# Kernel tuning notes

Measured on AMD Instinct MI355X. Metric: run time of the kernel, lower is better.

Reference implementation:

```python
import jax, jax.numpy as jnp
import numpy as np

B, L, D, H, R = 2, 2048, 1024, 16, 32
DH = D // H
LORA_SCALE = 64.0 / 32.0  # alpha / rank


def _ln(x, w, b):
    mu = jnp.mean(x, axis=-1, keepdims=True)
    xc = x - mu
    var = jnp.mean(xc * xc, axis=-1, keepdims=True)
    y = xc * jax.lax.rsqrt(var + 1e-5) * w
    return y + b if b is not None else y


def _rotate_half(x):
    x1, x2 = jnp.split(x, 2, axis=-1)
    return jnp.concatenate([-x2, x1], axis=-1)


def _apply_rotary(q, k):
    # q, k: [B, L, H, DH]
    seqlen = q.shape[1]
    inv_freq = 1.0 / (10000.0 ** (jnp.arange(0, DH, 2, dtype=jnp.float32) / DH))
    t = jnp.arange(seqlen, dtype=jnp.float32)
    freqs = t[:, None] * inv_freq[None, :]           # [L, DH/2]
    emb = jnp.concatenate([freqs, freqs], axis=-1)   # [L, DH]
    cos = jnp.cos(emb)[None, :, None, :]
    sin = jnp.sin(emb)[None, :, None, :]
    q = q * cos + _rotate_half(q) * sin
    k = k * cos + _rotate_half(k) * sin
    return q, k


def setup_inputs() -> dict:
    key = jax.random.key(0)
    ks = jax.random.split(key, 10)
    s = 0.02
    return {
        "x": jax.random.normal(ks[0], (B, L, D), dtype=jnp.float32),
        "seq_id": jnp.sort(jax.random.randint(ks[1], (B, L), 0, 4), axis=-1),
        "ln_w": jnp.ones((D,), jnp.float32),
        "ln_b": jnp.zeros((D,), jnp.float32),
        "w_qkv": jax.random.normal(ks[2], (3 * D, D), jnp.float32) * s,
        "q_lora_a": jax.random.normal(ks[3], (R, D), jnp.float32) * s,
        "q_lora_b": jax.random.normal(ks[4], (D, R), jnp.float32) * s,
        "v_lora_a": jax.random.normal(ks[5], (R, D), jnp.float32) * s,
        "v_lora_b": jax.random.normal(ks[6], (D, R), jnp.float32) * s,
        "q_ln_w": jnp.ones((D,), jnp.float32),
        "k_ln_w": jnp.ones((D,), jnp.float32),
        "w_out": jax.random.normal(ks[7], (D, D), jnp.float32) * s,
    }


def reference(x, seq_id, ln_w, ln_b, w_qkv, q_lora_a, q_lora_b,
              v_lora_a, v_lora_b, q_ln_w, k_ln_w, w_out):
    h = _ln(x, ln_w, ln_b)                          # [B, L, D]
    qkv = jnp.einsum('bld,ed->ble', h, w_qkv)       # [B, L, 3D]
    q, k, v = jnp.split(qkv, 3, axis=-1)
    q = q + LORA_SCALE * jnp.einsum('blr,dr->bld', jnp.einsum('bld,rd->blr', h, q_lora_a), q_lora_b)
    v = v + LORA_SCALE * jnp.einsum('blr,dr->bld', jnp.einsum('bld,rd->blr', h, v_lora_a), v_lora_b)
    q = _ln(q, q_ln_w, None)
    k = _ln(k, k_ln_w, None)
    q = q.reshape(B, L, H, DH)
    k = k.reshape(B, L, H, DH)
    q, k = _apply_rotary(q, k)
    qh = q.transpose(0, 2, 1, 3)                    # [B, H, L, DH]
    kh = k.transpose(0, 2, 1, 3)
    vh = v.reshape(B, L, H, DH).transpose(0, 2, 1, 3)
    scale = 1.0 / np.sqrt(DH)
    scores = jnp.einsum('bhqd,bhkd->bhqk', qh, kh) * scale
    mask = (seq_id[:, None, :, None] == seq_id[:, None, None, :])  # [B,1,L,L]
    scores = jnp.where(mask, scores, jnp.finfo(scores.dtype).min)
    attn = jax.nn.softmax(scores, axis=-1)
    ctx = jnp.einsum('bhqk,bhkd->bhqd', attn, vh)   # [B, H, L, DH]
    ctx = ctx.transpose(0, 2, 1, 3).reshape(B, L, D)
    return jnp.einsum('bld,ed->ble', ctx, w_out)
```

## Files before the change

kernel.cpp:

```cpp
#include <hip/hip_runtime.h>
#include <hip/hip_bf16.h>
#include <cmath>

constexpr int Bb = 2;
constexpr int Ls = 2048;
constexpr int Dd = 1024;
constexpr int Hh = 16;
constexpr int DHh = 64;
constexpr int Rr = 32;
constexpr int BL = Bb * Ls;
constexpr float LORA_SCALE = 2.0f;
constexpr float LN_EPS = 1e-5f;
constexpr float ATTN_SCALE = 0.125f;
constexpr float LOG2E = 1.4426950408889634f;
constexpr float QSCL = ATTN_SCALE * LOG2E;

typedef __attribute__((ext_vector_type(8))) short bf16x8;
typedef __attribute__((ext_vector_type(4))) float f32x4;

__device__ __forceinline__ unsigned short f2bf(float f) {
    __hip_bfloat16 b = __float2bfloat16(f);
    return *reinterpret_cast<unsigned short*>(&b);
}
__device__ __forceinline__ float bf2f(unsigned short u) {
    unsigned int x = ((unsigned int)u) << 16;
    return __uint_as_float(x);
}
__device__ __forceinline__ void async_copy16(const void* g, void* l) {
    __builtin_amdgcn_global_load_lds(
        (__attribute__((address_space(1))) void*)(void*)(size_t)g,
        (__attribute__((address_space(3))) void*)l, 16, 0, 0);
}

__device__ __forceinline__ float block_sum_256(float v, float* red) {
#pragma unroll
    for (int o = 32; o > 0; o >>= 1) v += __shfl_down(v, o, 64);
    const int lane = threadIdx.x & 63;
    const int wid = threadIdx.x >> 6;
    if (lane == 0) red[wid] = v;
    __syncthreads();
    float s = red[0] + red[1] + red[2] + red[3];
    __syncthreads();
    return s;
}

__global__ __launch_bounds__(256) void cast_bf16_kernel(const float* __restrict__ src,
                                                        unsigned short* __restrict__ dst,
                                                        int n) {
    int i = (blockIdx.x * 256 + threadIdx.x) * 4;
    if (i < n) {
        float4 v = *(const float4*)(src + i);
        ushort4 o;
        o.x = f2bf(v.x); o.y = f2bf(v.y); o.z = f2bf(v.z); o.w = f2bf(v.w);
        *(ushort4*)(dst + i) = o;
    }
}

__global__ __launch_bounds__(256) void merge_cast_wqkv(const float* __restrict__ w,
                                                       const float* __restrict__ qa,
                                                       const float* __restrict__ qb,
                                                       const float* __restrict__ va,
                                                       const float* __restrict__ vb,
                                                       unsigned short* __restrict__ dst) {
    const int e = blockIdx.x;
    const int tid = threadIdx.x;
    const int d0 = tid * 4;
    __shared__ float br[Rr];
    const bool isq = (e < Dd);
    const bool isv = (e >= 2 * Dd);
    const float* bsrc = isq ? (qb + (size_t)e * Rr)
                            : (isv ? (vb + (size_t)(e - 2 * Dd) * Rr) : nullptr);
    const float* asrc = isq ? qa : va;
    if (bsrc && tid < Rr) br[tid] = bsrc[tid];
    __syncthreads();
    float acc[4] = {0.f, 0.f, 0.f, 0.f};
    if (bsrc) {
#pragma unroll 8
        for (int r = 0; r < Rr; ++r) {
            float4 av = *(const float4*)(asrc + (size_t)r * Dd + d0);
            acc[0] += br[r] * av.x; acc[1] += br[r] * av.y;
            acc[2] += br[r] * av.z; acc[3] += br[r] * av.w;
        }
    }
    float4 wv = *(const float4*)(w + (size_t)e * Dd + d0);
    ushort4 o;
    o.x = f2bf(wv.x + LORA_SCALE * acc[0]);
    o.y = f2bf(wv.y + LORA_SCALE * acc[1]);
    o.z = f2bf(wv.z + LORA_SCALE * acc[2]);
    o.w = f2bf(wv.w + LORA_SCALE * acc[3]);
    *(ushort4*)(dst + (size_t)e * Dd + d0) = o;
}

__global__ __launch_bounds__(256) void rope_table_kernel(float* __restrict__ cs,
                                                         float* __restrict__ sn) {
    int i = blockIdx.x * 256 + threadIdx.x;
    int l = i >> 5;
    int f = i & 31;
    float invf = powf(10000.0f, -(float)f * (1.0f / 32.0f));
    float ang = (float)l * invf;
    float s, c;
    sincosf(ang, &s, &c);
    cs[i] = c;
    sn[i] = s;
}

__global__ __launch_bounds__(256) void ln_x_kernel(const float* __restrict__ x,
                                                   const float* __restrict__ w,
                                                   const float* __restrict__ b,
                                                   unsigned short* __restrict__ hb) {
    const int row = blockIdx.x;
    const int tid = threadIdx.x;
    __shared__ float red[4];
    float4 xv = *(const float4*)(x + (size_t)row * Dd + tid * 4);
    float v[4] = {xv.x, xv.y, xv.z, xv.w};
    float s = v[0] + v[1] + v[2] + v[3];
    float mean = block_sum_256(s, red) * (1.0f / Dd);
    float sq = 0.f;
#pragma unroll
    for (int j = 0; j < 4; ++j) {
        v[j] -= mean;
        sq += v[j] * v[j];
    }
    float var = block_sum_256(sq, red) * (1.0f / Dd);
    float rs = rsqrtf(var + LN_EPS);
    ushort4 o;
    unsigned short* op = (unsigned short*)&o;
#pragma unroll
    for (int j = 0; j < 4; ++j) {
        int d = tid * 4 + j;
        op[j] = f2bf(v[j] * rs * w[d] + b[d]);
    }
    *(ushort4*)(hb + (size_t)row * Dd + tid * 4) = o;
}

__global__ __launch_bounds__(256) void gemm_bt_mfma(const unsigned short* __restrict__ A,
                                                    const unsigned short* __restrict__ B,
                                                    float* __restrict__ C,
                                                    int M, int N, int K) {
    __shared__ short As[128 * 64];
    __shared__ short Bs[128 * 64];
    const int tid = threadIdx.x;
    const int w = tid >> 6, lane = tid & 63, quad = lane >> 4, l15 = lane & 15;
    const int m0 = blockIdx.y * 128, n0 = blockIdx.x * 128;
    const int wm = (w & 1) * 64, wn = (w >> 1) * 64;
    f32x4 acc[4][4];
#pragma unroll
    for (int i = 0; i < 4; ++i)
#pragma unroll
        for (int j = 0; j < 4; ++j) acc[i][j] = f32x4{0.f, 0.f, 0.f, 0.f};

    for (int k0 = 0; k0 < K; k0 += 64) {
#pragma unroll
        for (int j = 0; j < 4; ++j) {
            int c = tid + j * 256;
            int row = c >> 3;
            int jg = (c & 7) ^ (row & 7);
            async_copy16(A + (size_t)(m0 + row) * K + k0 + jg * 8, As + c * 8);
        }
#pragma unroll
        for (int j = 0; j < 4; ++j) {
            int c = tid + j * 256;
            int row = c >> 3;
            int jg = (c & 7) ^ (row & 7);
            async_copy16(B + (size_t)(n0 + row) * K + k0 + jg * 8, Bs + c * 8);
        }
        __syncthreads();
#pragma unroll
        for (int ks = 0; ks < 2; ++ks) {
            bf16x8 a[4], b[4];
#pragma unroll
            for (int mi = 0; mi < 4; ++mi) {
                int row = wm + mi * 16 + l15;
                int ch = (ks * 4 + quad) ^ (row & 7);
                a[mi] = *(const bf16x8*)&As[row * 64 + ch * 8];
            }
#pragma unroll
            for (int ni = 0; ni < 4; ++ni) {
                int row = wn + ni * 16 + l15;
                int ch = (ks * 4 + quad) ^ (row & 7);
                b[ni] = *(const bf16x8*)&Bs[row * 64 + ch * 8];
            }
#pragma unroll
            for (int mi = 0; mi < 4; ++mi)
#pragma unroll
                for (int ni = 0; ni < 4; ++ni)
                    acc[mi][ni] = __builtin_amdgcn_mfma_f32_16x16x32_bf16(a[mi], b[ni], acc[mi][ni], 0, 0, 0);
        }
        __syncthreads();
    }
#pragma unroll
    for (int mi = 0; mi < 4; ++mi)
#pragma unroll
        for (int ni = 0; ni < 4; ++ni)
#pragma unroll
            for (int r = 0; r < 4; ++r)
                C[(size_t)(m0 + wm + mi * 16 + quad * 4 + r) * N + n0 + wn + ni * 16 + l15] =
                    acc[mi][ni][r];
}

__global__ __launch_bounds__(256) void qkv_final_kernel(const float* __restrict__ qkv,
                                                        const float* __restrict__ qlnw,
                                                        const float* __restrict__ klnw,
                                                        const float* __restrict__ ropec,
                                                        const float* __restrict__ ropes,
                                                        unsigned short* __restrict__ qt,
                                                        unsigned short* __restrict__ kt) {
    const int row = blockIdx.x;
    const int b = row >> 11;
    const int l = row & (Ls - 1);
    const int tid = threadIdx.x;
    __shared__ float yrow[Dd];
    __shared__ float red[4];

    const int d0 = tid * 4;
    const int hh = d0 >> 6;
    const int dh0 = d0 & 63;
    float cs4[4], sn4[4];
#pragma unroll
    for (int j = 0; j < 4; ++j) {
        int f = (dh0 + j) & 31;
        cs4[j] = ropec[l * 32 + f];
        sn4[j] = ropes[l * 32 + f];
    }
    const size_t dst_off = (((size_t)(b * Hh + hh)) * Ls + l) * DHh + dh0;

    {
        float4 qv = *(const float4*)(qkv + (size_t)row * (3 * Dd) + d0);
        float v[4] = {qv.x, qv.y, qv.z, qv.w};
        float s = v[0] + v[1] + v[2] + v[3];
        float mean = block_sum_256(s, red) * (1.0f / Dd);
        float sq = 0.f;
#pragma unroll
        for (int j = 0; j < 4; ++j) {
            v[j] -= mean;
            sq += v[j] * v[j];
        }
        float var = block_sum_256(sq, red) * (1.0f / Dd);
        float rs = rsqrtf(var + LN_EPS);
#pragma unroll
        for (int j = 0; j < 4; ++j) yrow[d0 + j] = v[j] * rs * qlnw[d0 + j];
        __syncthreads();
        ushort4 pk;
        unsigned short* pp = (unsigned short*)&pk;
#pragma unroll
        for (int j = 0; j < 4; ++j) {
            int d = d0 + j;
            int dh = dh0 + j;
            float rot = (dh < 32) ? -yrow[d + 32] : yrow[d - 32];
            pp[j] = f2bf((yrow[d] * cs4[j] + rot * sn4[j]) * QSCL);
        }
        *(ushort4*)(qt + dst_off) = pk;
    }
    __syncthreads();

    {
        float4 kv = *(const float4*)(qkv + (size_t)row * (3 * Dd) + Dd + d0);
        float v[4] = {kv.x, kv.y, kv.z, kv.w};
        float s = v[0] + v[1] + v[2] + v[3];
        float mean = block_sum_256(s, red) * (1.0f / Dd);
        float sq = 0.f;
#pragma unroll
        for (int j = 0; j < 4; ++j) {
            v[j] -= mean;
            sq += v[j] * v[j];
        }
        float var = block_sum_256(sq, red) * (1.0f / Dd);
        float rs = rsqrtf(var + LN_EPS);
#pragma unroll
        for (int j = 0; j < 4; ++j) yrow[d0 + j] = v[j] * rs * klnw[d0 + j];
        __syncthreads();
        ushort4 pk;
        unsigned short* pp = (unsigned short*)&pk;
#pragma unroll
        for (int j = 0; j < 4; ++j) {
            int d = d0 + j;
            int dh = dh0 + j;
            float rot = (dh < 32) ? -yrow[d + 32] : yrow[d - 32];
            pp[j] = f2bf(yrow[d] * cs4[j] + rot * sn4[j]);
        }
        *(ushort4*)(kt + dst_off) = pk;
    }
}

__global__ __launch_bounds__(256) void transpose_v_kernel(const float* __restrict__ qkv,
                                                          unsigned short* __restrict__ vtt) {
    const int l0 = blockIdx.x * 64;
    const int h = blockIdx.y;
    const int b = blockIdx.z;
    const int tid = threadIdx.x;
    __shared__ short t[64][72];
    const float* src = qkv + (size_t)b * Ls * (3 * Dd) + 2 * Dd + h * 64;
#pragma unroll
    for (int j = 0; j < 2; ++j) {
        int g = tid + j * 256;
        int row = g >> 3;
        int c0 = (g & 7) * 8;
        float4 v0 = *(const float4*)(src + (size_t)(l0 + row) * (3 * Dd) + c0);
        float4 v1 = *(const float4*)(src + (size_t)(l0 + row) * (3 * Dd) + c0 + 4);
        ushort4 o0, o1;
        o0.x = f2bf(v0.x); o0.y = f2bf(v0.y); o0.z = f2bf(v0.z); o0.w = f2bf(v0.w);
        o1.x = f2bf(v1.x); o1.y = f2bf(v1.y); o1.z = f2bf(v1.z); o1.w = f2bf(v1.w);
        *(ushort4*)&t[row][c0] = o0;
        *(ushort4*)&t[row][c0 + 4] = o1;
    }
    __syncthreads();
    unsigned short* dst = vtt + ((size_t)(b * Hh + h) * DHh) * Ls;
#pragma unroll
    for (int j = 0; j < 2; ++j) {
        int g = tid + j * 256;
        int dh = g >> 3;
        int lc = (g & 7) * 8;
        ushort4 o0, o1;
        unsigned short* p0 = (unsigned short*)&o0;
        unsigned short* p1 = (unsigned short*)&o1;
#pragma unroll
        for (int i = 0; i < 4; ++i) p0[i] = (unsigned short)t[lc + i][dh];
#pragma unroll
        for (int i = 0; i < 4; ++i) p1[i] = (unsigned short)t[lc + 4 + i][dh];
        *(ushort4*)(dst + (size_t)dh * Ls + l0 + lc) = o0;
        *(ushort4*)(dst + (size_t)dh * Ls + l0 + lc + 4) = o1;
    }
}

constexpr int PSP = 76;

__global__ __launch_bounds__(256) void attn_kernel(const unsigned short* __restrict__ qt,
                                                   const unsigned short* __restrict__ kt,
                                                   const unsigned short* __restrict__ vtt,
                                                   const int* __restrict__ seq_id,
                                                   unsigned short* __restrict__ ctxb) {
    const int id = blockIdx.x;
    const int c8 = id & 7;
    const int x = (id >> 3) & 31;
    const int g8 = id >> 8;
    const int v = c8 + 8 * g8;
    const int b = v >> 4;
    const int h = v & 15;
    const int q0 = x * 64;

    const size_t base = ((size_t)(b * Hh + h)) * Ls * DHh;
    const size_t base_v = ((size_t)(b * Hh + h)) * DHh * Ls;
    const int* sid = seq_id + (size_t)b * Ls;

    __shared__ short Qs[64 * 64];
    __shared__ short Ks[2][64 * 64];
    __shared__ short Vs[2][64 * 64];
    __shared__ short Ps[4][16 * PSP];
    __shared__ int sq_s[64];

    const int tid = threadIdx.x;
    const int w = tid >> 6;
    const int lane = tid & 63;
    const int quad = lane >> 4;
    const int l15 = lane & 15;

#pragma unroll
    for (int j = 0; j < 2; ++j) {
        int cc = tid + j * 256;
        int row = cc >> 3;
        int jg = (cc & 7) ^ (row & 7);
        async_copy16(qt + base + (size_t)(q0 + row) * DHh + jg * 8, Qs + cc * 8);
    }
    if (tid < 64) sq_s[tid] = sid[q0 + tid];
    const int qmin = sid[q0];
    const int qmax = sid[q0 + 63];

    bool need = false;
    if (lane < 32) {
        int kmn = sid[lane * 64];
        int kmx = sid[lane * 64 + 63];
        need = (kmn <= qmax) && (kmx >= qmin);
    }
    unsigned long long bmask = __ballot(need);
    const int t0 = __builtin_ctzll(bmask);
    const int t1 = 64 - __builtin_clzll(bmask);

    auto stage = [&](int t, int buf) {
        int k0 = t * 64;
#pragma unroll
        for (int j = 0; j < 2; ++j) {
            int cc = tid + j * 256;
            int row = cc >> 3;
            int jg = (cc & 7) ^ (row & 7);
            async_copy16(kt + base + (size_t)(k0 + row) * DHh + jg * 8, &Ks[buf][cc * 8]);
            async_copy16(vtt + base_v + (size_t)row * Ls + k0 + jg * 8, &Vs[buf][cc * 8]);
        }
    };

    stage(t0, 0);
    __syncthreads();

    float lsum[4] = {0.f, 0.f, 0.f, 0.f};
    f32x4 O[4];
#pragma unroll
    for (int r = 0; r < 4; ++r) O[r] = f32x4{0.f, 0.f, 0.f, 0.f};

    const int qrow = w * 16 + l15;
    bf16x8 a0 = *(const bf16x8*)&Qs[qrow * 64 + ((0 + quad) ^ (qrow & 7)) * 8];
    bf16x8 a1 = *(const bf16x8*)&Qs[qrow * 64 + ((4 + quad) ^ (qrow & 7)) * 8];

    int cur = 0;
    for (int t = t0; t < t1; ++t) {
        const int k0 = t * 64;
        if (t + 1 < t1) stage(t + 1, cur ^ 1);

        f32x4 s[4];
#pragma unroll
        for (int kg = 0; kg < 4; ++kg) {
            int krow = kg * 16 + l15;
            bf16x8 b0 = *(const bf16x8*)&Ks[cur][krow * 64 + ((0 + quad) ^ (krow & 7)) * 8];
            bf16x8 b1 = *(const bf16x8*)&Ks[cur][krow * 64 + ((4 + quad) ^ (krow & 7)) * 8];
            f32x4 acc = {0.f, 0.f, 0.f, 0.f};
            acc = __builtin_amdgcn_mfma_f32_16x16x32_bf16(a0, b0, acc, 0, 0, 0);
            acc = __builtin_amdgcn_mfma_f32_16x16x32_bf16(a1, b1, acc, 0, 0, 0);
            s[kg] = acc;
        }
        const int kmn = sid[k0];
        const int kmx = sid[k0 + 63];
        const bool nomask = (kmn == kmx) && (qmin == qmax) && (kmn == qmin);
        if (!nomask) {
            int sqv[4];
#pragma unroll
            for (int r = 0; r < 4; ++r) sqv[r] = sq_s[w * 16 + quad * 4 + r];
#pragma unroll
            for (int kg = 0; kg < 4; ++kg) {
                int skv = sid[k0 + kg * 16 + l15];
#pragma unroll
                for (int r = 0; r < 4; ++r)
                    if (sqv[r] != skv) s[kg][r] = -3.0e38f;
            }
        }
#pragma unroll
        for (int kg = 0; kg < 4; ++kg)
#pragma unroll
            for (int r = 0; r < 4; ++r)
                s[kg][r] = __builtin_amdgcn_exp2f(s[kg][r]);
#pragma unroll
        for (int r = 0; r < 4; ++r)
            lsum[r] += s[0][r] + s[1][r] + s[2][r] + s[3][r];
#pragma unroll
        for (int kg = 0; kg < 4; ++kg)
#pragma unroll
            for (int r = 0; r < 4; ++r)
                Ps[w][(quad * 4 + r) * PSP + kg * 16 + l15] = (short)f2bf(s[kg][r]);
        bf16x8 pa0 = *(const bf16x8*)&Ps[w][l15 * PSP + quad * 8];
        bf16x8 pa1 = *(const bf16x8*)&Ps[w][l15 * PSP + 32 + quad * 8];
#pragma unroll
        for (int ng = 0; ng < 4; ++ng) {
            int vrow = ng * 16 + l15;
            bf16x8 vb0 = *(const bf16x8*)&Vs[cur][vrow * 64 + ((0 + quad) ^ (vrow & 7)) * 8];
            bf16x8 vb1 = *(const bf16x8*)&Vs[cur][vrow * 64 + ((4 + quad) ^ (vrow & 7)) * 8];
            O[ng] = __builtin_amdgcn_mfma_f32_16x16x32_bf16(pa0, vb0, O[ng], 0, 0, 0);
            O[ng] = __builtin_amdgcn_mfma_f32_16x16x32_bf16(pa1, vb1, O[ng], 0, 0, 0);
        }
        __syncthreads();
        cur ^= 1;
    }

#pragma unroll
    for (int off = 1; off < 16; off <<= 1)
#pragma unroll
        for (int r = 0; r < 4; ++r)
            lsum[r] += __shfl_xor(lsum[r], off, 64);
    float inv_l[4];
#pragma unroll
    for (int r = 0; r < 4; ++r) inv_l[r] = 1.0f / lsum[r];
#pragma unroll
    for (int ng = 0; ng < 4; ++ng)
#pragma unroll
        for (int r = 0; r < 4; ++r) {
            int q = q0 + w * 16 + quad * 4 + r;
            ctxb[((size_t)b * Ls + q) * Dd + h * DHh + ng * 16 + l15] = f2bf(O[ng][r] * inv_l[r]);
        }
}

extern "C" void kernel_launch(void* const* d_in, const int* in_sizes, int n_in,
                              void* d_out, int out_size, void* d_ws, size_t ws_size,
                              hipStream_t stream) {
    const float* x = (const float*)d_in[0];
    const int* seq_id = (const int*)d_in[1];
    const float* ln_w = (const float*)d_in[2];
    const float* ln_b = (const float*)d_in[3];
    const float* w_qkv = (const float*)d_in[4];
    const float* q_lora_a = (const float*)d_in[5];
    const float* q_lora_b = (const float*)d_in[6];
    const float* v_lora_a = (const float*)d_in[7];
    const float* v_lora_b = (const float*)d_in[8];
    const float* q_ln_w = (const float*)d_in[9];
    const float* k_ln_w = (const float*)d_in[10];
    const float* w_out = (const float*)d_in[11];
    float* out = (float*)d_out;

    const size_t SZ = (size_t)BL * Dd;
    float* p = (float*)d_ws;
    float* qkv = p;            p += 3 * SZ;
    float* ropec = p;          p += (size_t)Ls * 32;
    float* ropes = p;          p += (size_t)Ls * 32;
    unsigned short* ub = (unsigned short*)p;
    unsigned short* hb = ub;   ub += SZ;
    unsigned short* qt = ub;   ub += SZ;
    unsigned short* kt = ub;   ub += SZ;
    unsigned short* vtt = ub;  ub += SZ;
    unsigned short* ctxb = ub; ub += SZ;
    unsigned short* wqkvb = ub; ub += (size_t)3 * Dd * Dd;
    unsigned short* woutb = ub; ub += (size_t)Dd * Dd;

    rope_table_kernel<<<(Ls * 32) / 256, 256, 0, stream>>>(ropec, ropes);
    merge_cast_wqkv<<<3 * Dd, 256, 0, stream>>>(w_qkv, q_lora_a, q_lora_b,
                                                v_lora_a, v_lora_b, wqkvb);
    cast_bf16_kernel<<<(Dd * Dd) / 1024, 256, 0, stream>>>(w_out, woutb, Dd * Dd);
    ln_x_kernel<<<BL, 256, 0, stream>>>(x, ln_w, ln_b, hb);
    {
        dim3 g(3 * Dd / 128, BL / 128);
        gemm_bt_mfma<<<g, 256, 0, stream>>>(hb, wqkvb, qkv, BL, 3 * Dd, Dd);
    }
    qkv_final_kernel<<<BL, 256, 0, stream>>>(qkv, q_ln_w, k_ln_w,
                                             ropec, ropes, qt, kt);
    {
        dim3 g(Ls / 64, Hh, Bb);
        transpose_v_kernel<<<g, 256, 0, stream>>>(qkv, vtt);
    }
    attn_kernel<<<1024, 256, 0, stream>>>(qt, kt, vtt, seq_id, ctxb);
    {
        dim3 g(Dd / 128, BL / 128);
        gemm_bt_mfma<<<g, 256, 0, stream>>>(ctxb, woutb, out, BL, Dd, Dd);
    }
}
```

Measured before the change: 236.9 us.

## Store QKV GEMM output as bf16 and merge weight-prep kernels into one

The QKV projection GEMM now writes bf16 instead of fp32. That halves the intermediate traffic for the write and for the later reads in qkv_final and transpose_v, and the transpose becomes a plain 16-byte copy. Separately, the rope-table, merged LoRA weight cast and w_out cast kernels are combined into a single launch to save launch overhead. Q and K are now rounded to bf16 before their layernorm, which adds some precision loss.

```diff
diff --git a/kernel.cpp b/kernel.cpp
--- a/kernel.cpp
+++ b/kernel.cpp
@@ -44,64 +44,62 @@
     return s;
 }
 
-__global__ __launch_bounds__(256) void cast_bf16_kernel(const float* __restrict__ src,
-                                                        unsigned short* __restrict__ dst,
-                                                        int n) {
-    int i = (blockIdx.x * 256 + threadIdx.x) * 4;
-    if (i < n) {
-        float4 v = *(const float4*)(src + i);
+__global__ __launch_bounds__(256) void prep_kernel(const float* __restrict__ w,
+                                                   const float* __restrict__ qa,
+                                                   const float* __restrict__ qb,
+                                                   const float* __restrict__ va,
+                                                   const float* __restrict__ vb,
+                                                   const float* __restrict__ wout,
+                                                   unsigned short* __restrict__ wqkvb,
+                                                   unsigned short* __restrict__ woutb,
+                                                   float* __restrict__ ropec,
+                                                   float* __restrict__ ropes) {
+    const int blk = blockIdx.x;
+    const int tid = threadIdx.x;
+    if (blk < 3 * Dd) {
+        const int e = blk;
+        const int d0 = tid * 4;
+        __shared__ float br[Rr];
+        const bool isq = (e < Dd);
+        const bool isv = (e >= 2 * Dd);
+        const float* bsrc = isq ? (qb + (size_t)e * Rr)
+                                : (isv ? (vb + (size_t)(e - 2 * Dd) * Rr) : nullptr);
+        const float* asrc = isq ? qa : va;
+        if (bsrc && tid < Rr) br[tid] = bsrc[tid];
+        __syncthreads();
+        float acc[4] = {0.f, 0.f, 0.f, 0.f};
+        if (bsrc) {
+#pragma unroll 8
+            for (int r = 0; r < Rr; ++r) {
+                float4 av = *(const float4*)(asrc + (size_t)r * Dd + d0);
+                acc[0] += br[r] * av.x; acc[1] += br[r] * av.y;
+                acc[2] += br[r] * av.z; acc[3] += br[r] * av.w;
+            }
+        }
+        float4 wv = *(const float4*)(w + (size_t)e * Dd + d0);
+        ushort4 o;
+        o.x = f2bf(wv.x + LORA_SCALE * acc[0]);
+        o.y = f2bf(wv.y + LORA_SCALE * acc[1]);
+        o.z = f2bf(wv.z + LORA_SCALE * acc[2]);
+        o.w = f2bf(wv.w + LORA_SCALE * acc[3]);
+        *(ushort4*)(wqkvb + (size_t)e * Dd + d0) = o;
+    } else if (blk < 4 * Dd) {
+        int i = ((blk - 3 * Dd) * 256 + tid) * 4;
+        float4 v = *(const float4*)(wout + i);
         ushort4 o;
         o.x = f2bf(v.x); o.y = f2bf(v.y); o.z = f2bf(v.z); o.w = f2bf(v.w);
-        *(ushort4*)(dst + i) = o;
-    }
-}
-
-__global__ __launch_bounds__(256) void merge_cast_wqkv(const float* __restrict__ w,
-                                                       const float* __restrict__ qa,
-                                                       const float* __restrict__ qb,
-                                                       const float* __restrict__ va,
-                                                       const float* __restrict__ vb,
-                                                       unsigned short* __restrict__ dst) {
-    const int e = blockIdx.x;
-    const int tid = threadIdx.x;
-    const int d0 = tid * 4;
-    __shared__ float br[Rr];
-    const bool isq = (e < Dd);
-    const bool isv = (e >= 2 * Dd);
-    const float* bsrc = isq ? (qb + (size_t)e * Rr)
-                            : (isv ? (vb + (size_t)(e - 2 * Dd) * Rr) : nullptr);
-    const float* asrc = isq ? qa : va;
-    if (bsrc && tid < Rr) br[tid] = bsrc[tid];
-    __syncthreads();
-    float acc[4] = {0.f, 0.f, 0.f, 0.f};
-    if (bsrc) {
-#pragma unroll 8
-        for (int r = 0; r < Rr; ++r) {
-            float4 av = *(const float4*)(asrc + (size_t)r * Dd + d0);
-            acc[0] += br[r] * av.x; acc[1] += br[r] * av.y;
-            acc[2] += br[r] * av.z; acc[3] += br[r] * av.w;
-        }
-    }
-    float4 wv = *(const float4*)(w + (size_t)e * Dd + d0);
-    ushort4 o;
-    o.x = f2bf(wv.x + LORA_SCALE * acc[0]);
-    o.y = f2bf(wv.y + LORA_SCALE * acc[1]);
-    o.z = f2bf(wv.z + LORA_SCALE * acc[2]);
-    o.w = f2bf(wv.w + LORA_SCALE * acc[3]);
-    *(ushort4*)(dst + (size_t)e * Dd + d0) = o;
-}
-
-__global__ __launch_bounds__(256) void rope_table_kernel(float* __restrict__ cs,
-                                                         float* __restrict__ sn) {
-    int i = blockIdx.x * 256 + threadIdx.x;
-    int l = i >> 5;
-    int f = i & 31;
-    float invf = powf(10000.0f, -(float)f * (1.0f / 32.0f));
-    float ang = (float)l * invf;
-    float s, c;
-    sincosf(ang, &s, &c);
-    cs[i] = c;
-    sn[i] = s;
+        *(ushort4*)(woutb + i) = o;
+    } else {
+        int i = (blk - 4 * Dd) * 256 + tid;
+        int l = i >> 5;
+        int f = i & 31;
+        float invf = powf(10000.0f, -(float)f * (1.0f / 32.0f));
+        float ang = (float)l * invf;
+        float s, c;
+        sincosf(ang, &s, &c);
+        ropec[i] = c;
+        ropes[i] = s;
+    }
 }
 
 __global__ __launch_bounds__(256) void ln_x_kernel(const float* __restrict__ x,
@@ -133,9 +131,10 @@
     *(ushort4*)(hb + (size_t)row * Dd + tid * 4) = o;
 }
 
+template <bool OUT_BF16>
 __global__ __launch_bounds__(256) void gemm_bt_mfma(const unsigned short* __restrict__ A,
                                                     const unsigned short* __restrict__ B,
-                                                    float* __restrict__ C,
+                                                    void* __restrict__ Cv,
                                                     int M, int N, int K) {
     __shared__ short As[128 * 64];
     __shared__ short Bs[128 * 64];
@@ -188,17 +187,30 @@
         }
         __syncthreads();
     }
-#pragma unroll
-    for (int mi = 0; mi < 4; ++mi)
-#pragma unroll
-        for (int ni = 0; ni < 4; ++ni)
-#pragma unroll
-            for (int r = 0; r < 4; ++r)
-                C[(size_t)(m0 + wm + mi * 16 + quad * 4 + r) * N + n0 + wn + ni * 16 + l15] =
-                    acc[mi][ni][r];
-}
-
-__global__ __launch_bounds__(256) void qkv_final_kernel(const float* __restrict__ qkv,
+    if (OUT_BF16) {
+        unsigned short* C = (unsigned short*)Cv;
+#pragma unroll
+        for (int mi = 0; mi < 4; ++mi)
+#pragma unroll
+            for (int ni = 0; ni < 4; ++ni)
+#pragma unroll
+                for (int r = 0; r < 4; ++r)
+                    C[(size_t)(m0 + wm + mi * 16 + quad * 4 + r) * N + n0 + wn + ni * 16 + l15] =
+                        f2bf(acc[mi][ni][r]);
+    } else {
+        float* C = (float*)Cv;
+#pragma unroll
+        for (int mi = 0; mi < 4; ++mi)
+#pragma unroll
+            for (int ni = 0; ni < 4; ++ni)
+#pragma unroll
+                for (int r = 0; r < 4; ++r)
+                    C[(size_t)(m0 + wm + mi * 16 + quad * 4 + r) * N + n0 + wn + ni * 16 + l15] =
+                        acc[mi][ni][r];
+    }
+}
+
+__global__ __launch_bounds__(256) void qkv_final_kernel(const unsigned short* __restrict__ qkvb,
                                                         const float* __restrict__ qlnw,
                                                         const float* __restrict__ klnw,
                                                         const float* __restrict__ ropec,
@@ -225,8 +237,8 @@
     const size_t dst_off = (((size_t)(b * Hh + hh)) * Ls + l) * DHh + dh0;
 
     {
-        float4 qv = *(const float4*)(qkv + (size_t)row * (3 * Dd) + d0);
-        float v[4] = {qv.x, qv.y, qv.z, qv.w};
+        ushort4 qv = *(const ushort4*)(qkvb + (size_t)row * (3 * Dd) + d0);
+        float v[4] = {bf2f(qv.x), bf2f(qv.y), bf2f(qv.z), bf2f(qv.w)};
         float s = v[0] + v[1] + v[2] + v[3];
         float mean = block_sum_256(s, red) * (1.0f / Dd);
         float sq = 0.f;
@@ -254,8 +266,8 @@
     __syncthreads();
 
     {
-        float4 kv = *(const float4*)(qkv + (size_t)row * (3 * Dd) + Dd + d0);
-        float v[4] = {kv.x, kv.y, kv.z, kv.w};
+        ushort4 kv = *(const ushort4*)(qkvb + (size_t)row * (3 * Dd) + Dd + d0);
+        float v[4] = {bf2f(kv.x), bf2f(kv.y), bf2f(kv.z), bf2f(kv.w)};
         float s = v[0] + v[1] + v[2] + v[3];
         float mean = block_sum_256(s, red) * (1.0f / Dd);
         float sq = 0.f;
@@ -282,26 +294,21 @@
     }
 }
 
-__global__ __launch_bounds__(256) void transpose_v_kernel(const float* __restrict__ qkv,
+__global__ __launch_bounds__(256) void transpose_v_kernel(const unsigned short* __restrict__ qkvb,
                                                           unsigned short* __restrict__ vtt) {
     const int l0 = blockIdx.x * 64;
     const int h = blockIdx.y;
     const int b = blockIdx.z;
     const int tid = threadIdx.x;
     __shared__ short t[64][72];
-    const float* src = qkv + (size_t)b * Ls * (3 * Dd) + 2 * Dd + h * 64;
+    const unsigned short* src = qkvb + (size_t)b * Ls * (3 * Dd) + 2 * Dd + h * 64;
 #pragma unroll
     for (int j = 0; j < 2; ++j) {
         int g = tid + j * 256;
         int row = g >> 3;
         int c0 = (g & 7) * 8;
-        float4 v0 = *(const float4*)(src + (size_t)(l0 + row) * (3 * Dd) + c0);
-        float4 v1 = *(const float4*)(src + (size_t)(l0 + row) * (3 * Dd) + c0 + 4);
-        ushort4 o0, o1;
-        o0.x = f2bf(v0.x); o0.y = f2bf(v0.y); o0.z = f2bf(v0.z); o0.w = f2bf(v0.w);
-        o1.x = f2bf(v1.x); o1.y = f2bf(v1.y); o1.z = f2bf(v1.z); o1.w = f2bf(v1.w);
-        *(ushort4*)&t[row][c0] = o0;
-        *(ushort4*)&t[row][c0 + 4] = o1;
+        uint4 vv = *(const uint4*)(src + (size_t)(l0 + row) * (3 * Dd) + c0);
+        *(uint4*)&t[row][c0] = vv;
     }
     __syncthreads();
     unsigned short* dst = vtt + ((size_t)(b * Hh + h) * DHh) * Ls;
@@ -493,10 +500,10 @@
 
     const size_t SZ = (size_t)BL * Dd;
     float* p = (float*)d_ws;
-    float* qkv = p;            p += 3 * SZ;
     float* ropec = p;          p += (size_t)Ls * 32;
     float* ropes = p;          p += (size_t)Ls * 32;
     unsigned short* ub = (unsigned short*)p;
+    unsigned short* qkvb = ub; ub += 3 * SZ;
     unsigned short* hb = ub;   ub += SZ;
     unsigned short* qt = ub;   ub += SZ;
     unsigned short* kt = ub;   ub += SZ;
@@ -505,24 +512,23 @@
     unsigned short* wqkvb = ub; ub += (size_t)3 * Dd * Dd;
     unsigned short* woutb = ub; ub += (size_t)Dd * Dd;
 
-    rope_table_kernel<<<(Ls * 32) / 256, 256, 0, stream>>>(ropec, ropes);
-    merge_cast_wqkv<<<3 * Dd, 256, 0, stream>>>(w_qkv, q_lora_a, q_lora_b,
-                                                v_lora_a, v_lora_b, wqkvb);
-    cast_bf16_kernel<<<(Dd * Dd) / 1024, 256, 0, stream>>>(w_out, woutb, Dd * Dd);
+    prep_kernel<<<4 * Dd + 256, 256, 0, stream>>>(w_qkv, q_lora_a, q_lora_b,
+                                                  v_lora_a, v_lora_b, w_out,
+                                                  wqkvb, woutb, ropec, ropes);
     ln_x_kernel<<<BL, 256, 0, stream>>>(x, ln_w, ln_b, hb);
     {
         dim3 g(3 * Dd / 128, BL / 128);
-        gemm_bt_mfma<<<g, 256, 0, stream>>>(hb, wqkvb, qkv, BL, 3 * Dd, Dd);
-    }
-    qkv_final_kernel<<<BL, 256, 0, stream>>>(qkv, q_ln_w, k_ln_w,
+        gemm_bt_mfma<true><<<g, 256, 0, stream>>>(hb, wqkvb, qkvb, BL, 3 * Dd, Dd);
+    }
+    qkv_final_kernel<<<BL, 256, 0, stream>>>(qkvb, q_ln_w, k_ln_w,
                                              ropec, ropes, qt, kt);
     {
         dim3 g(Ls / 64, Hh, Bb);
-        transpose_v_kernel<<<g, 256, 0, stream>>>(qkv, vtt);
+        transpose_v_kernel<<<g, 256, 0, stream>>>(qkvb, vtt);
     }
     attn_kernel<<<1024, 256, 0, stream>>>(qt, kt, vtt, seq_id, ctxb);
     {
         dim3 g(Dd / 128, BL / 128);
-        gemm_bt_mfma<<<g, 256, 0, stream>>>(ctxb, woutb, out, BL, Dd, Dd);
-    }
-}
+        gemm_bt_mfma<false><<<g, 256, 0, stream>>>(ctxb, woutb, out, BL, Dd, Dd);
+    }
+}
```

Measured after the change: 223.0 us. -5.9%, faster.
